# Kernel optimization log

Measured on AMD Instinct MI355X. Metric: run time of the kernel, lower is better.

## Reference

```python
import jax, jax.numpy as jnp
import numpy as np

N_NODES = 100000
N_EDGES = 800000
D_NODE = 64          # node_channels
D_EDGE = 4           # edge_feature_dim (2*layer_idx+2, layer 1)
H_MSG = 128          # message_hidden_channels
H_UPD = 128          # update_hidden_channels


def setup_inputs() -> dict:
    key = jax.random.key(0)
    ks = jax.random.split(key, 9)
    s = 0.05  # small init scale for numerical stability
    return {
        "x": jax.random.normal(ks[0], (N_NODES, D_NODE), dtype=jnp.float32),
        "edge_index": jax.random.randint(ks[1], (2, N_EDGES), 0, N_NODES, dtype=jnp.int32),
        "edge_features": jax.random.uniform(ks[2], (N_EDGES, D_EDGE), dtype=jnp.float32),
        "W1": jax.random.normal(ks[3], (2 * D_NODE + D_EDGE, H_MSG), dtype=jnp.float32) * s,
        "b1": jnp.zeros((H_MSG,), dtype=jnp.float32),
        "W2": jax.random.normal(ks[4], (H_MSG, D_NODE), dtype=jnp.float32) * s,
        "b2": jnp.zeros((D_NODE,), dtype=jnp.float32),
        "U1": jax.random.normal(ks[5], (2 * D_NODE, H_UPD), dtype=jnp.float32) * s,
        "bu1": jnp.zeros((H_UPD,), dtype=jnp.float32),
        "U2": jax.random.normal(ks[6], (H_UPD, D_NODE), dtype=jnp.float32) * s,
        "bu2": jnp.zeros((D_NODE,), dtype=jnp.float32),
    }


def reference(x, edge_index, edge_features, W1, b1, W2, b2, U1, bu1, U2, bu2):
    src, dst = edge_index[0], edge_index[1]
    # message phase: gather endpoints, log1p edge feats, concat, 2-layer MLP
    ef = jnp.log1p(edge_features)                       # [E, D_EDGE]
    msg_in = jnp.concatenate([x[src], x[dst], ef], axis=-1)  # [E, 2D+De]
    messages = jax.nn.relu(msg_in @ W1 + b1) @ W2 + b2  # [E, D_NODE]
    # aggregate: scatter-add into destination nodes
    agg = jnp.zeros_like(x).at[dst].add(messages)       # [N, D_NODE]
    # update phase
    upd_in = jnp.concatenate([x, agg], axis=-1)         # [N, 2*D_NODE]
    return jax.nn.relu(upd_in @ U1 + bu1) @ U2 + bu2    # [N, D_NODE]
```

## Files before the change

kernel.cpp:

```cpp
#include <hip/hip_runtime.h>
#include <math.h>

#define NN 100000
#define NE 800000
#define DN 64
#define DE 4
#define HH 128
#define NT 64
#define NT2 64
#define SCAN_B 256
#define NBLK_SCAN ((NN + SCAN_B - 1) / SCAN_B)

using bf16x8 = __attribute__((ext_vector_type(8))) short;
using f32x4  = __attribute__((ext_vector_type(4))) float;

__device__ __forceinline__ unsigned short f2bf(float f) {
    unsigned int u = __float_as_uint(f);
    unsigned int r = (u + 0x7fffu + ((u >> 16) & 1u)) >> 16;
    return (unsigned short)r;
}
__device__ __forceinline__ float bf2f(unsigned short h) {
    return __uint_as_float(((unsigned int)h) << 16);
}
__device__ __forceinline__ float2 bfpair2f(unsigned int v) {
    return make_float2(__uint_as_float(v << 16),
                       __uint_as_float(v & 0xffff0000u));
}

__global__ __launch_bounds__(256) void k_xproj(const float* __restrict__ x,
                                               const unsigned short* __restrict__ Wpx,
                                               unsigned short* __restrict__ XAb,
                                               float* __restrict__ XB) {
    __shared__ unsigned short sA[8 * 64 * 8];
    const int n0 = blockIdx.x * NT;
    const int t  = threadIdx.x;
    const int w    = t >> 6;
    const int l    = t & 63;
    const int quad = l >> 4;
    const int l16  = l & 15;

#pragma unroll
    for (int it = 0; it < 4; ++it) {
        const int flat = t + it * 256;
        const int node = flat >> 4;
        const int c    = flat & 15;
        const int gn   = n0 + node;
        float4 v = make_float4(0.f, 0.f, 0.f, 0.f);
        if (gn < NN) v = *(const float4*)(x + (size_t)gn * DN + c * 4);
        const int k = c * 4, Q = k >> 3, j0 = k & 7;
        uint2 pk;
        pk.x = (unsigned)f2bf(v.x) | ((unsigned)f2bf(v.y) << 16);
        pk.y = (unsigned)f2bf(v.z) | ((unsigned)f2bf(v.w) << 16);
        *(uint2*)(&sA[(Q * 64 + node) * 8 + j0]) = pk;
    }
    __syncthreads();

    const int mrow = w * 16 + l16;
    f32x4 acc[16];
#pragma unroll
    for (int nt = 0; nt < 16; ++nt) { acc[nt][0] = 0.f; acc[nt][1] = 0.f; acc[nt][2] = 0.f; acc[nt][3] = 0.f; }

#pragma unroll
    for (int kb = 0; kb < 2; ++kb) {
        bf16x8 a = *(const bf16x8*)(const void*)(&sA[((kb * 4 + quad) * 64 + mrow) * 8]);
#pragma unroll
        for (int nt = 0; nt < 16; ++nt) {
            bf16x8 b = *(const bf16x8*)(const void*)(Wpx + ((size_t)(nt * 2 + kb) * 64 + l) * 8);
            acc[nt] = __builtin_amdgcn_mfma_f32_16x16x32_bf16(a, b, acc[nt], 0, 0, 0);
        }
    }
#pragma unroll
    for (int nt = 0; nt < 8; ++nt) {
        const int col = nt * 16 + l16;
#pragma unroll
        for (int r = 0; r < 4; ++r) {
            const int gn = n0 + w * 16 + quad * 4 + r;
            if (gn < NN) XAb[(size_t)gn * HH + col] = f2bf(acc[nt][r]);
        }
    }
#pragma unroll
    for (int nt = 8; nt < 16; ++nt) {
        const int col = (nt - 8) * 16 + l16;
#pragma unroll
        for (int r = 0; r < 4; ++r) {
            const int gn = n0 + w * 16 + quad * 4 + r;
            if (gn < NN) XB[(size_t)gn * HH + col] = acc[nt][r];
        }
    }
}

__global__ __launch_bounds__(256) void k_fold(const float* __restrict__ W2,
                                              const float* __restrict__ U1,
                                              const float* __restrict__ b2,
                                              float* __restrict__ Wc,
                                              float* __restrict__ cvec) {
    const int idx = blockIdx.x * 256 + threadIdx.x;
    const float* u1b = U1 + (size_t)DN * HH;
    if (blockIdx.x < 64) {
        const int r = idx >> 7;
        const int c = idx & 127;
        float acc = 0.f;
#pragma unroll 8
        for (int j = 0; j < DN; ++j)
            acc = fmaf(W2[(size_t)r * DN + j], u1b[(size_t)j * HH + c], acc);
        Wc[(size_t)r * HH + c] = acc;
    } else if (threadIdx.x < HH) {
        const int c = threadIdx.x;
        float acc = 0.f;
#pragma unroll 8
        for (int j = 0; j < DN; ++j)
            acc = fmaf(b2[j], u1b[(size_t)j * HH + c], acc);
        cvec[c] = acc;
    }
}

__global__ __launch_bounds__(256) void k_pack(const float* __restrict__ U1,
                                              const float* __restrict__ Wc,
                                              const float* __restrict__ U2,
                                              const float* __restrict__ W1,
                                              unsigned short* __restrict__ Wpa,
                                              unsigned short* __restrict__ Wpb,
                                              unsigned short* __restrict__ Wpx) {
    const int tid = blockIdx.x * 256 + threadIdx.x;
    if (tid < 3072) {
        const int l  = tid & 63;
        const int kb = (tid >> 6) % 6;
        const int n  = tid / 384;
        const int kbase = kb * 32 + (l >> 4) * 8;
        const int col   = n * 16 + (l & 15);
        unsigned short tmp[8];
#pragma unroll
        for (int j = 0; j < 8; ++j) {
            const int k = kbase + j;
            const float v = (k < DN) ? U1[(size_t)k * HH + col]
                                     : Wc[(size_t)(k - DN) * HH + col];
            tmp[j] = f2bf(v);
        }
        *(uint4*)(Wpa + (size_t)tid * 8) = *(const uint4*)tmp;
    } else if (tid < 4096) {
        const int t2 = tid - 3072;
        const int l  = t2 & 63;
        const int kb = (t2 >> 6) & 3;
        const int n2 = t2 >> 8;
        const int kbase = kb * 32 + (l >> 4) * 8;
        const int col   = n2 * 16 + (l & 15);
        unsigned short tmp[8];
#pragma unroll
        for (int j = 0; j < 8; ++j) tmp[j] = f2bf(U2[(size_t)(kbase + j) * DN + col]);
        *(uint4*)(Wpb + (size_t)t2 * 8) = *(const uint4*)tmp;
    } else if (tid < 6144) {
        const int t3 = tid - 4096;
        const int l  = t3 & 63;
        const int kb = (t3 >> 6) & 1;
        const int nt = t3 >> 7;
        const int kbase = kb * 32 + (l >> 4) * 8;
        const int row0  = (nt < 8) ? 0 : DN;
        const int col   = ((nt & 7) * 16) + (l & 15);
        unsigned short tmp[8];
#pragma unroll
        for (int j = 0; j < 8; ++j)
            tmp[j] = f2bf(W1[(size_t)(row0 + kbase + j) * HH + col]);
        *(uint4*)(Wpx + (size_t)t3 * 8) = *(const uint4*)tmp;
    }
}

__global__ __launch_bounds__(256) void k_hist(const int* __restrict__ ei,
                                              int* __restrict__ cnt) {
    const int e = blockIdx.x * 256 + threadIdx.x;
    if (e < NE) atomicAdd(&cnt[ei[NE + e]], 1);
}

__global__ __launch_bounds__(SCAN_B) void k_scan_a(const int* __restrict__ cnt,
                                                   int* __restrict__ pos,
                                                   int* __restrict__ bsum) {
    __shared__ int sh[SCAN_B];
    const int n = blockIdx.x * SCAN_B + threadIdx.x;
    const int c = (n < NN) ? cnt[n] : 0;
    sh[threadIdx.x] = c;
    __syncthreads();
    int v = c;
#pragma unroll
    for (int off = 1; off < SCAN_B; off <<= 1) {
        int add = (threadIdx.x >= off) ? sh[threadIdx.x - off] : 0;
        __syncthreads();
        v += add;
        sh[threadIdx.x] = v;
        __syncthreads();
    }
    if (n < NN) pos[n] = v - c;
    if (threadIdx.x == SCAN_B - 1) bsum[blockIdx.x] = v;
}

__global__ __launch_bounds__(512) void k_scan_b(int* __restrict__ bsum) {
    __shared__ int sh[512];
    const int i = threadIdx.x;
    const int c = (i < NBLK_SCAN) ? bsum[i] : 0;
    sh[i] = c;
    __syncthreads();
    int v = c;
#pragma unroll
    for (int off = 1; off < 512; off <<= 1) {
        int add = (i >= off) ? sh[i - off] : 0;
        __syncthreads();
        v += add;
        sh[i] = v;
        __syncthreads();
    }
    if (i < NBLK_SCAN) bsum[i] = v - c;
}

__global__ __launch_bounds__(256) void k_scatter(const int* __restrict__ ei,
                                                 const float* __restrict__ ef,
                                                 int* __restrict__ pos,
                                                 const int* __restrict__ boff,
                                                 int* __restrict__ es,
                                                 float4* __restrict__ ef4) {
    const int e = blockIdx.x * 256 + threadIdx.x;
    if (e >= NE) return;
    const int s = ei[e];
    const int d = ei[NE + e];
    const int slot = atomicAdd(&pos[d], 1) + boff[d >> 8];
    es[slot] = s;
    ef4[slot] = make_float4(log1pf(ef[e * 4 + 0]), log1pf(ef[e * 4 + 1]),
                            log1pf(ef[e * 4 + 2]), log1pf(ef[e * 4 + 3]));
}

#define EDGE_COMPUTE(ff, aa)                                     \
    {                                                            \
        const float2 av = bfpair2f(aa);                          \
        float h0 = av.x + base0;                                 \
        float h1 = av.y + base1;                                 \
        h0 = fmaf(ff.x, wv0.x, h0); h0 = fmaf(ff.y, wv1.x, h0);  \
        h0 = fmaf(ff.z, wv2.x, h0); h0 = fmaf(ff.w, wv3.x, h0);  \
        h1 = fmaf(ff.x, wv0.y, h1); h1 = fmaf(ff.y, wv1.y, h1);  \
        h1 = fmaf(ff.z, wv2.y, h1); h1 = fmaf(ff.w, wv3.y, h1);  \
        acc0 += fmaxf(h0, 0.f);                                  \
        acc1 += fmaxf(h1, 0.f);                                  \
    }

__global__ __launch_bounds__(256) void k_agg(const int* __restrict__ es,
                                             const float4* __restrict__ ef4,
                                             const int* __restrict__ pos,
                                             const int* __restrict__ boff,
                                             const int* __restrict__ cnt,
                                             const unsigned short* __restrict__ XAb,
                                             const float* __restrict__ XB,
                                             const float* __restrict__ W1,
                                             const float* __restrict__ b1,
                                             unsigned short* __restrict__ Haggb,
                                             float* __restrict__ deg) {
    const int wave = threadIdx.x >> 6;
    const int lane = threadIdx.x & 63;
    const int d = blockIdx.x * 4 + wave;
    if (d >= NN) return;
    const int c     = cnt[d];
    const int end   = pos[d] + boff[d >> 8];
    const int start = end - c;
    const int j0    = lane * 2;

    const float* we = W1 + 128 * HH;
    const float2 xb = *(const float2*)(XB + (size_t)d * HH + j0);
    const float2 bb = *(const float2*)(b1 + j0);
    const float base0 = xb.x + bb.x;
    const float base1 = xb.y + bb.y;
    const float2 wv0 = *(const float2*)(we + 0 * HH + j0);
    const float2 wv1 = *(const float2*)(we + 1 * HH + j0);
    const float2 wv2 = *(const float2*)(we + 2 * HH + j0);
    const float2 wv3 = *(const float2*)(we + 3 * HH + j0);

    float acc0 = 0.f, acc1 = 0.f;
    if (c > 0) {
        float4 s0f = make_float4(0.f, 0.f, 0.f, 0.f);
        float4 s1f = s0f, s2f = s0f, s3f = s0f;
        unsigned s0a = 0u, s1a = 0u, s2a = 0u, s3a = 0u;

        s0f = ef4[start];
        s0a = *(const unsigned*)(XAb + (size_t)es[start] * HH + j0);
        if (c > 1) {
            s1f = ef4[start + 1];
            s1a = *(const unsigned*)(XAb + (size_t)es[start + 1] * HH + j0);
        }
        if (c > 2) {
            s2f = ef4[start + 2];
            s2a = *(const unsigned*)(XAb + (size_t)es[start + 2] * HH + j0);
        }
        if (c > 3) {
            s3f = ef4[start + 3];
            s3a = *(const unsigned*)(XAb + (size_t)es[start + 3] * HH + j0);
        }

        int k = start;
        for (; k + 1 < end; k += 2) {
            const float4 f0 = s0f; const unsigned a0 = s0a;
            const float4 f1 = s1f; const unsigned a1 = s1a;
            s0f = s2f; s0a = s2a;
            s1f = s3f; s1a = s3a;
            if (k + 4 < end) {
                s2f = ef4[k + 4];
                s2a = *(const unsigned*)(XAb + (size_t)es[k + 4] * HH + j0);
            }
            if (k + 5 < end) {
                s3f = ef4[k + 5];
                s3a = *(const unsigned*)(XAb + (size_t)es[k + 5] * HH + j0);
            }
            EDGE_COMPUTE(f0, a0);
            EDGE_COMPUTE(f1, a1);
        }
        if (k < end) EDGE_COMPUTE(s0f, s0a);
    }
    const unsigned int p = (unsigned)f2bf(acc0) | ((unsigned)f2bf(acc1) << 16);
    *(unsigned int*)(Haggb + (size_t)d * HH + j0) = p;
    if (lane == 0) deg[d] = (float)c;
}

__global__ __launch_bounds__(256) void k_edge_atomic(const int* __restrict__ ei,
                                                     const float* __restrict__ ef,
                                                     const float* __restrict__ W1,
                                                     const float* __restrict__ b1,
                                                     const unsigned short* __restrict__ XAb,
                                                     const float* __restrict__ XB,
                                                     float* __restrict__ Hagg,
                                                     float* __restrict__ deg) {
    const int wave = threadIdx.x >> 6;
    const int lane = threadIdx.x & 63;
    const long e = (long)blockIdx.x * 4 + wave;
    if (e >= NE) return;
    const int s = ei[e];
    const int d = ei[NE + e];

    float t = 0.f;
    if (lane < DE) t = log1pf(ef[e * DE + lane]);
    const float l0 = __shfl(t, 0);
    const float l1 = __shfl(t, 1);
    const float l2 = __shfl(t, 2);
    const float l3 = __shfl(t, 3);

    const float* we = W1 + 128 * HH;
    const size_t sb = (size_t)s * HH;
    const size_t db = (size_t)d * HH;
#pragma unroll
    for (int r = 0; r < 2; ++r) {
        const int j = lane + r * 64;
        float h = bf2f(XAb[sb + j]) + XB[db + j] + b1[j];
        h = fmaf(l0, we[0 * HH + j], h);
        h = fmaf(l1, we[1 * HH + j], h);
        h = fmaf(l2, we[2 * HH + j], h);
        h = fmaf(l3, we[3 * HH + j], h);
        h = fmaxf(h, 0.f);
        atomicAdd(&Hagg[db + j], h);
    }
    if (lane == 0) atomicAdd(&deg[d], 1.f);
}

__global__ __launch_bounds__(256) void k_update(const float* __restrict__ x,
                                                const void* __restrict__ HaggV,
                                                const int hbf16,
                                                const float* __restrict__ deg,
                                                const unsigned short* __restrict__ Wpa,
                                                const unsigned short* __restrict__ Wpb,
                                                const float* __restrict__ cvec,
                                                const float* __restrict__ bu1,
                                                const float* __restrict__ bu2,
                                                float* __restrict__ out) {
    __shared__ unsigned short sA[6 * 4 * 64 * 8];
    __shared__ float sdeg[NT2];
    const int n0 = blockIdx.x * NT2;
    const int t  = threadIdx.x;
    const int w    = t >> 6;
    const int l    = t & 63;
    const int quad = l >> 4;
    const int l16  = l & 15;

#pragma unroll
    for (int it = 0; it < 4; ++it) {
        const int flat = t + it * 256;
        const int node = flat >> 4;
        const int c    = flat & 15;
        const int gn   = n0 + node;
        float4 v = make_float4(0.f, 0.f, 0.f, 0.f);
        if (gn < NN) v = *(const float4*)(x + (size_t)gn * DN + c * 4);
        const int k = c * 4, Q = k >> 3, j0 = k & 7;
        uint2 pk;
        pk.x = (unsigned)f2bf(v.x) | ((unsigned)f2bf(v.y) << 16);
        pk.y = (unsigned)f2bf(v.z) | ((unsigned)f2bf(v.w) << 16);
        *(uint2*)(&sA[(Q * 64 + node) * 8 + j0]) = pk;
    }
    if (hbf16) {
        const unsigned short* Hb = (const unsigned short*)HaggV;
#pragma unroll
        for (int it = 0; it < 4; ++it) {
            const int flat = t + it * 256;
            const int node = flat >> 4;
            const int c8   = flat & 15;
            const int gn   = n0 + node;
            uint4 v = make_uint4(0u, 0u, 0u, 0u);
            if (gn < NN) v = *(const uint4*)(Hb + (size_t)gn * HH + c8 * 8);
            const int Q = 8 + c8;
            *(uint4*)(&sA[(Q * 64 + node) * 8]) = v;
        }
    } else {
        const float* Hagg = (const float*)HaggV;
#pragma unroll
        for (int it = 0; it < 8; ++it) {
            const int flat = t + it * 256;
            const int node = flat >> 5;
            const int c    = flat & 31;
            const int gn   = n0 + node;
            float4 v = make_float4(0.f, 0.f, 0.f, 0.f);
            if (gn < NN) v = *(const float4*)(Hagg + (size_t)gn * HH + c * 4);
            const int k = DN + c * 4, Q = k >> 3, j0 = k & 7;
            uint2 pk;
            pk.x = (unsigned)f2bf(v.x) | ((unsigned)f2bf(v.y) << 16);
            pk.y = (unsigned)f2bf(v.z) | ((unsigned)f2bf(v.w) << 16);
            *(uint2*)(&sA[(Q * 64 + node) * 8 + j0]) = pk;
        }
    }
    if (t < NT2) sdeg[t] = (n0 + t < NN) ? deg[n0 + t] : 0.f;
    __syncthreads();

    f32x4 acc[8];
#pragma unroll
    for (int n = 0; n < 8; ++n) {
        const int col = n * 16 + l16;
        const float bv = bu1[col];
        const float cv = cvec[col];
#pragma unroll
        for (int r = 0; r < 4; ++r)
            acc[n][r] = fmaf(sdeg[w * 16 + quad * 4 + r], cv, bv);
    }
    const int mrow = w * 16 + l16;
#pragma unroll
    for (int kb = 0; kb < 6; ++kb) {
        bf16x8 a = *(const bf16x8*)(const void*)(&sA[((kb * 4 + quad) * 64 + mrow) * 8]);
#pragma unroll
        for (int n = 0; n < 8; ++n) {
            bf16x8 b = *(const bf16x8*)(const void*)(Wpa + ((size_t)(n * 6 + kb) * 64 + l) * 8);
            acc[n] = __builtin_amdgcn_mfma_f32_16x16x32_bf16(a, b, acc[n], 0, 0, 0);
        }
    }
    __syncthreads();

#pragma unroll
    for (int n = 0; n < 8; ++n) {
        const int col = n * 16 + l16;
        const int Q = col >> 3;
        const int j = col & 7;
#pragma unroll
        for (int r = 0; r < 4; ++r) {
            const int m = w * 16 + quad * 4 + r;
            sA[(Q * 64 + m) * 8 + j] = f2bf(fmaxf(acc[n][r], 0.f));
        }
    }
    __syncthreads();

    f32x4 acc2[4];
#pragma unroll
    for (int n2 = 0; n2 < 4; ++n2) {
        const float bv = bu2[n2 * 16 + l16];
        acc2[n2][0] = bv; acc2[n2][1] = bv; acc2[n2][2] = bv; acc2[n2][3] = bv;
    }
#pragma unroll
    for (int kb = 0; kb < 4; ++kb) {
        bf16x8 a = *(const bf16x8*)(const void*)(&sA[((kb * 4 + quad) * 64 + mrow) * 8]);
#pragma unroll
        for (int n2 = 0; n2 < 4; ++n2) {
            bf16x8 b = *(const bf16x8*)(const void*)(Wpb + ((size_t)(n2 * 4 + kb) * 64 + l) * 8);
            acc2[n2] = __builtin_amdgcn_mfma_f32_16x16x32_bf16(a, b, acc2[n2], 0, 0, 0);
        }
    }
#pragma unroll
    for (int n2 = 0; n2 < 4; ++n2) {
        const int col = n2 * 16 + l16;
#pragma unroll
        for (int r = 0; r < 4; ++r) {
            const int gn = n0 + w * 16 + quad * 4 + r;
            if (gn < NN) out[(size_t)gn * DN + col] = acc2[n2][r];
        }
    }
}

extern "C" void kernel_launch(void* const* d_in, const int* in_sizes, int n_in,
                              void* d_out, int out_size, void* d_ws, size_t ws_size,
                              hipStream_t stream) {
    const float* x   = (const float*)d_in[0];
    const int*   ei  = (const int*)d_in[1];
    const float* ef  = (const float*)d_in[2];
    const float* W1  = (const float*)d_in[3];
    const float* b1  = (const float*)d_in[4];
    const float* W2  = (const float*)d_in[5];
    const float* b2  = (const float*)d_in[6];
    const float* U1  = (const float*)d_in[7];
    const float* bu1 = (const float*)d_in[8];
    const float* U2  = (const float*)d_in[9];
    const float* bu2 = (const float*)d_in[10];
    float* out = (float*)d_out;

    unsigned short* XAb = (unsigned short*)d_ws;
    float* XB   = (float*)(XAb + (size_t)NN * HH);
    float* Hagg = XB + (size_t)NN * HH;
    float* deg  = Hagg + (size_t)NN * HH;
    float* Wc   = deg + NN;
    float* cvec = Wc + (size_t)HH * HH;
    unsigned short* Wpa = (unsigned short*)(cvec + HH);
    unsigned short* Wpb = Wpa + 8 * 6 * 64 * 8;
    unsigned short* Wpx = Wpb + 4 * 4 * 64 * 8;
    int*   cnt  = (int*)(Wpx + 16 * 2 * 64 * 8);
    int*   pos  = cnt + NN;
    int*   boff = pos + NN;
    int*   es   = boff + 1024;
    float4* ef4 = (float4*)(es + NE);
    const size_t need = (size_t)((char*)(ef4 + NE) - (char*)d_ws);

    unsigned short* Haggb = (unsigned short*)Hagg;

    const int nblk  = (NN + NT - 1) / NT;
    const int nblk2 = (NN + NT2 - 1) / NT2;

    k_fold<<<65, 256, 0, stream>>>(W2, U1, b2, Wc, cvec);
    k_pack<<<24, 256, 0, stream>>>(U1, Wc, U2, W1, Wpa, Wpb, Wpx);

    if (ws_size >= need) {
        hipMemsetAsync(cnt, 0, (size_t)NN * sizeof(int), stream);
        k_xproj<<<nblk, 256, 0, stream>>>(x, Wpx, XAb, XB);
        k_hist<<<(NE + 255) / 256, 256, 0, stream>>>(ei, cnt);
        k_scan_a<<<NBLK_SCAN, SCAN_B, 0, stream>>>(cnt, pos, boff);
        k_scan_b<<<1, 512, 0, stream>>>(boff);
        k_scatter<<<(NE + 255) / 256, 256, 0, stream>>>(ei, ef, pos, boff, es, ef4);
        k_agg<<<(NN + 3) / 4, 256, 0, stream>>>(es, ef4, pos, boff, cnt, XAb, XB, W1, b1, Haggb, deg);
        k_update<<<nblk2, 256, 0, stream>>>(x, (const void*)Haggb, 1, deg, Wpa, Wpb, cvec, bu1, bu2, out);
    } else {
        hipMemsetAsync(Hagg, 0, ((size_t)NN * HH + NN) * sizeof(float), stream);
        k_xproj<<<nblk, 256, 0, stream>>>(x, Wpx, XAb, XB);
        k_edge_atomic<<<NE / 4, 256, 0, stream>>>(ei, ef, W1, b1, XAb, XB, Hagg, deg);
        k_update<<<nblk2, 256, 0, stream>>>(x, (const void*)Hagg, 0, deg, Wpa, Wpb, cvec, bu1, bu2, out);
    }
}
```

Measured before the change: 327.5 us.

## Stage stores through LDS, fuse fold into pack, deepen edge gather prefetch

Output writes in k_xproj and k_update are staged through shared memory so each row goes to global memory with 16-byte coalesced stores instead of scattered scalar stores. The separate k_fold launch is removed and its W2·U1 fold and cvec work is computed inside k_pack. k_scatter now stores byte offsets for source rows, and k_agg uses an 8-deep software-pipelined prefetch of gathered rows and edge features, padding es with EPAD entries so reads past the end stay in bounds. The changes add extra syncthreads and LDS use, repeat the fold computation per packed element, and raise register pressure in the aggregation loop.

```diff
diff --git a/kernel.cpp b/kernel.cpp
--- a/kernel.cpp
+++ b/kernel.cpp
@@ -10,6 +10,7 @@
 #define NT2 64
 #define SCAN_B 256
 #define NBLK_SCAN ((NN + SCAN_B - 1) / SCAN_B)
+#define EPAD 16
 
 using bf16x8 = __attribute__((ext_vector_type(8))) short;
 using f32x4  = __attribute__((ext_vector_type(4))) float;
@@ -31,7 +32,9 @@
                                                const unsigned short* __restrict__ Wpx,
                                                unsigned short* __restrict__ XAb,
                                                float* __restrict__ XB) {
-    __shared__ unsigned short sA[8 * 64 * 8];
+    __shared__ __align__(16) float smemF[64 * 132];
+    unsigned short* sA  = (unsigned short*)smemF;
+    unsigned short* sXA = (unsigned short*)smemF;
     const int n0 = blockIdx.x * NT;
     const int t  = threadIdx.x;
     const int w    = t >> 6;
@@ -69,59 +72,57 @@
             acc[nt] = __builtin_amdgcn_mfma_f32_16x16x32_bf16(a, b, acc[nt], 0, 0, 0);
         }
     }
+    __syncthreads();
+
 #pragma unroll
     for (int nt = 0; nt < 8; ++nt) {
         const int col = nt * 16 + l16;
 #pragma unroll
-        for (int r = 0; r < 4; ++r) {
-            const int gn = n0 + w * 16 + quad * 4 + r;
-            if (gn < NN) XAb[(size_t)gn * HH + col] = f2bf(acc[nt][r]);
-        }
-    }
+        for (int r = 0; r < 4; ++r)
+            sXA[(w * 16 + quad * 4 + r) * 136 + col] = f2bf(acc[nt][r]);
+    }
+    __syncthreads();
+#pragma unroll
+    for (int it = 0; it < 4; ++it) {
+        const int idx  = t + it * 256;
+        const int node = idx >> 4;
+        const int u    = idx & 15;
+        const uint4 v  = *(const uint4*)(sXA + node * 136 + u * 8);
+        const int gn   = n0 + node;
+        if (gn < NN) *(uint4*)(XAb + (size_t)gn * HH + u * 8) = v;
+    }
+    __syncthreads();
+
 #pragma unroll
     for (int nt = 8; nt < 16; ++nt) {
         const int col = (nt - 8) * 16 + l16;
 #pragma unroll
-        for (int r = 0; r < 4; ++r) {
-            const int gn = n0 + w * 16 + quad * 4 + r;
-            if (gn < NN) XB[(size_t)gn * HH + col] = acc[nt][r];
-        }
-    }
-}
-
-__global__ __launch_bounds__(256) void k_fold(const float* __restrict__ W2,
-                                              const float* __restrict__ U1,
-                                              const float* __restrict__ b2,
-                                              float* __restrict__ Wc,
-                                              float* __restrict__ cvec) {
-    const int idx = blockIdx.x * 256 + threadIdx.x;
-    const float* u1b = U1 + (size_t)DN * HH;
-    if (blockIdx.x < 64) {
-        const int r = idx >> 7;
-        const int c = idx & 127;
-        float acc = 0.f;
-#pragma unroll 8
-        for (int j = 0; j < DN; ++j)
-            acc = fmaf(W2[(size_t)r * DN + j], u1b[(size_t)j * HH + c], acc);
-        Wc[(size_t)r * HH + c] = acc;
-    } else if (threadIdx.x < HH) {
-        const int c = threadIdx.x;
-        float acc = 0.f;
-#pragma unroll 8
-        for (int j = 0; j < DN; ++j)
-            acc = fmaf(b2[j], u1b[(size_t)j * HH + c], acc);
-        cvec[c] = acc;
+        for (int r = 0; r < 4; ++r)
+            smemF[(w * 16 + quad * 4 + r) * 132 + col] = acc[nt][r];
+    }
+    __syncthreads();
+#pragma unroll
+    for (int it = 0; it < 8; ++it) {
+        const int idx  = t + it * 256;
+        const int node = idx >> 5;
+        const int u    = idx & 31;
+        const uint4 v  = *(const uint4*)((const float*)smemF + node * 132 + u * 4);
+        const int gn   = n0 + node;
+        if (gn < NN) *(uint4*)(XB + (size_t)gn * HH + u * 4) = v;
     }
 }
 
 __global__ __launch_bounds__(256) void k_pack(const float* __restrict__ U1,
-                                              const float* __restrict__ Wc,
                                               const float* __restrict__ U2,
                                               const float* __restrict__ W1,
+                                              const float* __restrict__ W2,
+                                              const float* __restrict__ b2,
                                               unsigned short* __restrict__ Wpa,
                                               unsigned short* __restrict__ Wpb,
-                                              unsigned short* __restrict__ Wpx) {
+                                              unsigned short* __restrict__ Wpx,
+                                              float* __restrict__ cvec) {
     const int tid = blockIdx.x * 256 + threadIdx.x;
+    const float* u1b = U1 + (size_t)DN * HH;
     if (tid < 3072) {
         const int l  = tid & 63;
         const int kb = (tid >> 6) % 6;
@@ -132,8 +133,16 @@
 #pragma unroll
         for (int j = 0; j < 8; ++j) {
             const int k = kbase + j;
-            const float v = (k < DN) ? U1[(size_t)k * HH + col]
-                                     : Wc[(size_t)(k - DN) * HH + col];
+            float v;
+            if (k < DN) {
+                v = U1[(size_t)k * HH + col];
+            } else {
+                float a = 0.f;
+#pragma unroll 8
+                for (int jj = 0; jj < DN; ++jj)
+                    a = fmaf(W2[(size_t)(k - DN) * DN + jj], u1b[(size_t)jj * HH + col], a);
+                v = a;
+            }
             tmp[j] = f2bf(v);
         }
         *(uint4*)(Wpa + (size_t)tid * 8) = *(const uint4*)tmp;
@@ -161,13 +170,22 @@
         for (int j = 0; j < 8; ++j)
             tmp[j] = f2bf(W1[(size_t)(row0 + kbase + j) * HH + col]);
         *(uint4*)(Wpx + (size_t)t3 * 8) = *(const uint4*)tmp;
+    } else if (tid < 6272) {
+        const int cc = tid - 6144;
+        float a = 0.f;
+#pragma unroll 8
+        for (int jj = 0; jj < DN; ++jj)
+            a = fmaf(b2[jj], u1b[(size_t)jj * HH + cc], a);
+        cvec[cc] = a;
     }
 }
 
 __global__ __launch_bounds__(256) void k_hist(const int* __restrict__ ei,
-                                              int* __restrict__ cnt) {
+                                              int* __restrict__ cnt,
+                                              int* __restrict__ es) {
     const int e = blockIdx.x * 256 + threadIdx.x;
     if (e < NE) atomicAdd(&cnt[ei[NE + e]], 1);
+    if (blockIdx.x == 0 && threadIdx.x < EPAD) es[NE + threadIdx.x] = 0;
 }
 
 __global__ __launch_bounds__(SCAN_B) void k_scan_a(const int* __restrict__ cnt,
@@ -220,7 +238,7 @@
     const int s = ei[e];
     const int d = ei[NE + e];
     const int slot = atomicAdd(&pos[d], 1) + boff[d >> 8];
-    es[slot] = s;
+    es[slot] = s * (HH * 2);
     ef4[slot] = make_float4(log1pf(ef[e * 4 + 0]), log1pf(ef[e * 4 + 1]),
                             log1pf(ef[e * 4 + 2]), log1pf(ef[e * 4 + 3]));
 }
@@ -257,6 +275,7 @@
     const int end   = pos[d] + boff[d >> 8];
     const int start = end - c;
     const int j0    = lane * 2;
+    const unsigned jb = (unsigned)(lane * 4);
 
     const float* we = W1 + 128 * HH;
     const float2 xb = *(const float2*)(XB + (size_t)d * HH + j0);
@@ -270,43 +289,48 @@
 
     float acc0 = 0.f, acc1 = 0.f;
     if (c > 0) {
-        float4 s0f = make_float4(0.f, 0.f, 0.f, 0.f);
-        float4 s1f = s0f, s2f = s0f, s3f = s0f;
-        unsigned s0a = 0u, s1a = 0u, s2a = 0u, s3a = 0u;
-
-        s0f = ef4[start];
-        s0a = *(const unsigned*)(XAb + (size_t)es[start] * HH + j0);
-        if (c > 1) {
-            s1f = ef4[start + 1];
-            s1a = *(const unsigned*)(XAb + (size_t)es[start + 1] * HH + j0);
-        }
-        if (c > 2) {
-            s2f = ef4[start + 2];
-            s2a = *(const unsigned*)(XAb + (size_t)es[start + 2] * HH + j0);
-        }
-        if (c > 3) {
-            s3f = ef4[start + 3];
-            s3a = *(const unsigned*)(XAb + (size_t)es[start + 3] * HH + j0);
-        }
+        const char* XAc = (const char*)XAb;
+        int eA0 = es[start + 0], eA1 = es[start + 1], eA2 = es[start + 2], eA3 = es[start + 3];
+        int eB0 = es[start + 4], eB1 = es[start + 5], eB2 = es[start + 6], eB3 = es[start + 7];
+        unsigned aA0 = *(const unsigned*)(XAc + (unsigned)eA0 + jb);
+        unsigned aA1 = *(const unsigned*)(XAc + (unsigned)eA1 + jb);
+        unsigned aA2 = *(const unsigned*)(XAc + (unsigned)eA2 + jb);
+        unsigned aA3 = *(const unsigned*)(XAc + (unsigned)eA3 + jb);
+        float4 fA0 = ef4[start + 0], fA1 = ef4[start + 1], fA2 = ef4[start + 2], fA3 = ef4[start + 3];
+        unsigned aB0 = *(const unsigned*)(XAc + (unsigned)eB0 + jb);
+        unsigned aB1 = *(const unsigned*)(XAc + (unsigned)eB1 + jb);
+        unsigned aB2 = *(const unsigned*)(XAc + (unsigned)eB2 + jb);
+        unsigned aB3 = *(const unsigned*)(XAc + (unsigned)eB3 + jb);
+        float4 fB0 = ef4[start + 4], fB1 = ef4[start + 5], fB2 = ef4[start + 6], fB3 = ef4[start + 7];
+        eA0 = es[start + 8];  eA1 = es[start + 9];  eA2 = es[start + 10]; eA3 = es[start + 11];
+        eB0 = es[start + 12]; eB1 = es[start + 13]; eB2 = es[start + 14]; eB3 = es[start + 15];
 
         int k = start;
-        for (; k + 1 < end; k += 2) {
-            const float4 f0 = s0f; const unsigned a0 = s0a;
-            const float4 f1 = s1f; const unsigned a1 = s1a;
-            s0f = s2f; s0a = s2a;
-            s1f = s3f; s1a = s3a;
-            if (k + 4 < end) {
-                s2f = ef4[k + 4];
-                s2a = *(const unsigned*)(XAb + (size_t)es[k + 4] * HH + j0);
-            }
-            if (k + 5 < end) {
-                s3f = ef4[k + 5];
-                s3a = *(const unsigned*)(XAb + (size_t)es[k + 5] * HH + j0);
-            }
-            EDGE_COMPUTE(f0, a0);
-            EDGE_COMPUTE(f1, a1);
-        }
-        if (k < end) EDGE_COMPUTE(s0f, s0a);
+        while (true) {
+            EDGE_COMPUTE(fA0, aA0);
+            if (k + 1 < end) EDGE_COMPUTE(fA1, aA1);
+            if (k + 2 < end) EDGE_COMPUTE(fA2, aA2);
+            if (k + 3 < end) EDGE_COMPUTE(fA3, aA3);
+            if (k + 4 >= end) break;
+            aA0 = *(const unsigned*)(XAc + (unsigned)eA0 + jb);
+            aA1 = *(const unsigned*)(XAc + (unsigned)eA1 + jb);
+            aA2 = *(const unsigned*)(XAc + (unsigned)eA2 + jb);
+            aA3 = *(const unsigned*)(XAc + (unsigned)eA3 + jb);
+            fA0 = ef4[k + 8]; fA1 = ef4[k + 9]; fA2 = ef4[k + 10]; fA3 = ef4[k + 11];
+            eA0 = es[k + 16]; eA1 = es[k + 17]; eA2 = es[k + 18]; eA3 = es[k + 19];
+            EDGE_COMPUTE(fB0, aB0);
+            if (k + 5 < end) EDGE_COMPUTE(fB1, aB1);
+            if (k + 6 < end) EDGE_COMPUTE(fB2, aB2);
+            if (k + 7 < end) EDGE_COMPUTE(fB3, aB3);
+            if (k + 8 >= end) break;
+            aB0 = *(const unsigned*)(XAc + (unsigned)eB0 + jb);
+            aB1 = *(const unsigned*)(XAc + (unsigned)eB1 + jb);
+            aB2 = *(const unsigned*)(XAc + (unsigned)eB2 + jb);
+            aB3 = *(const unsigned*)(XAc + (unsigned)eB3 + jb);
+            fB0 = ef4[k + 12]; fB1 = ef4[k + 13]; fB2 = ef4[k + 14]; fB3 = ef4[k + 15];
+            eB0 = es[k + 20]; eB1 = es[k + 21]; eB2 = es[k + 22]; eB3 = es[k + 23];
+            k += 8;
+        }
     }
     const unsigned int p = (unsigned)f2bf(acc0) | ((unsigned)f2bf(acc1) << 16);
     *(unsigned int*)(Haggb + (size_t)d * HH + j0) = p;
@@ -362,7 +386,7 @@
                                                 const float* __restrict__ bu1,
                                                 const float* __restrict__ bu2,
                                                 float* __restrict__ out) {
-    __shared__ unsigned short sA[6 * 4 * 64 * 8];
+    __shared__ __align__(16) unsigned short sA[6 * 4 * 64 * 8];
     __shared__ float sdeg[NT2];
     const int n0 = blockIdx.x * NT2;
     const int t  = threadIdx.x;
@@ -468,14 +492,25 @@
             acc2[n2] = __builtin_amdgcn_mfma_f32_16x16x32_bf16(a, b, acc2[n2], 0, 0, 0);
         }
     }
+    __syncthreads();
+
+    float* sOut = (float*)sA;
 #pragma unroll
     for (int n2 = 0; n2 < 4; ++n2) {
         const int col = n2 * 16 + l16;
 #pragma unroll
-        for (int r = 0; r < 4; ++r) {
-            const int gn = n0 + w * 16 + quad * 4 + r;
-            if (gn < NN) out[(size_t)gn * DN + col] = acc2[n2][r];
-        }
+        for (int r = 0; r < 4; ++r)
+            sOut[(w * 16 + quad * 4 + r) * 68 + col] = acc2[n2][r];
+    }
+    __syncthreads();
+#pragma unroll
+    for (int it = 0; it < 4; ++it) {
+        const int idx  = t + it * 256;
+        const int node = idx >> 4;
+        const int u    = idx & 15;
+        const uint4 v  = *(const uint4*)(sOut + node * 68 + u * 4);
+        const int gn   = n0 + node;
+        if (gn < NN) *(uint4*)(out + (size_t)gn * DN + u * 4) = v;
     }
 }
 
@@ -508,21 +543,20 @@
     int*   pos  = cnt + NN;
     int*   boff = pos + NN;
     int*   es   = boff + 1024;
-    float4* ef4 = (float4*)(es + NE);
-    const size_t need = (size_t)((char*)(ef4 + NE) - (char*)d_ws);
+    float4* ef4 = (float4*)(es + NE + EPAD);
+    const size_t need = (size_t)((char*)(ef4 + NE + EPAD) - (char*)d_ws);
 
     unsigned short* Haggb = (unsigned short*)Hagg;
 
     const int nblk  = (NN + NT - 1) / NT;
     const int nblk2 = (NN + NT2 - 1) / NT2;
 
-    k_fold<<<65, 256, 0, stream>>>(W2, U1, b2, Wc, cvec);
-    k_pack<<<24, 256, 0, stream>>>(U1, Wc, U2, W1, Wpa, Wpb, Wpx);
+    k_pack<<<25, 256, 0, stream>>>(U1, U2, W1, W2, b2, Wpa, Wpb, Wpx, cvec);
 
     if (ws_size >= need) {
         hipMemsetAsync(cnt, 0, (size_t)NN * sizeof(int), stream);
         k_xproj<<<nblk, 256, 0, stream>>>(x, Wpx, XAb, XB);
-        k_hist<<<(NE + 255) / 256, 256, 0, stream>>>(ei, cnt);
+        k_hist<<<(NE + 255) / 256, 256, 0, stream>>>(ei, cnt, es);
         k_scan_a<<<NBLK_SCAN, SCAN_B, 0, stream>>>(cnt, pos, boff);
         k_scan_b<<<1, 512, 0, stream>>>(boff);
         k_scatter<<<(NE + 255) / 256, 256, 0, stream>>>(ei, ef, pos, boff, es, ef4);
```

Measured after the change: 369.1 us. +12.7%, slower.
